# Performance work log

Hardware: AMD Instinct MI355X
Metric: run time of the kernel (lower is better)

The kernel has to match this reference:

```python
import jax, jax.numpy as jnp
import numpy as np

N_HEAD = 16
N_EMBD = 1024
HEAD_DIM = N_EMBD // N_HEAD  # 64
ROPE_BASE = 10000.0


def _rotary_cos_sin(T, dim, dtype=jnp.float32):
    # matches Rotary: inv_freq over even indices, cos/sin cached in bfloat16
    inv_freq = 1.0 / (ROPE_BASE ** (jnp.arange(0, dim, 2, dtype=jnp.float32) / dim))
    freqs = jnp.arange(T, dtype=jnp.float32)[:, None] * inv_freq[None, :]  # [T, dim/2]
    cos = jnp.cos(freqs).astype(jnp.bfloat16).astype(dtype)
    sin = jnp.sin(freqs).astype(jnp.bfloat16).astype(dtype)
    # shape [1, T, 1, dim/2] to broadcast over (B, T, H, d)
    return cos[None, :, None, :], sin[None, :, None, :]


def _apply_rotary(x, cos, sin):
    d = x.shape[3] // 2
    x1, x2 = x[..., :d], x[..., d:]
    y1 = x1 * cos + x2 * sin
    y2 = -x1 * sin + x2 * cos
    return jnp.concatenate([y1, y2], axis=3).astype(x.dtype)


def setup_inputs() -> dict:
    key = jax.random.key(0)
    ks = jax.random.split(key, 8)
    B, T, C = 2, 2048, N_EMBD
    scale = C ** -0.5  # realistic linear-layer init scale
    x = jax.random.normal(ks[0], (B, T, C), dtype=jnp.float32)
    Wq1 = jax.random.normal(ks[1], (C, C), dtype=jnp.float32) * scale
    Wk1 = jax.random.normal(ks[2], (C, C), dtype=jnp.float32) * scale
    Wq2 = jax.random.normal(ks[3], (C, C), dtype=jnp.float32) * scale
    Wk2 = jax.random.normal(ks[4], (C, C), dtype=jnp.float32) * scale
    Wv = jax.random.normal(ks[5], (C, C), dtype=jnp.float32) * scale
    Wout = jax.random.normal(ks[6], (C, C), dtype=jnp.float32) * scale
    return {"x": x, "Wq1": Wq1, "Wk1": Wk1, "Wq2": Wq2, "Wk2": Wk2, "Wv": Wv, "Wout": Wout}


def reference(x, Wq1, Wk1, Wq2, Wk2, Wv, Wout):
    B, T, C = x.shape
    H, D = N_HEAD, HEAD_DIM

    def proj(W):
        # torch nn.Linear(bias=False): y = x @ W.T
        return (x @ W.T).reshape(B, T, H, D)

    q1, k1 = proj(Wq1), proj(Wk1)
    q2, k2 = proj(Wq2), proj(Wk2)
    v = proj(Wv)

    cos, sin = _rotary_cos_sin(T, D, x.dtype)
    q1, k1 = _apply_rotary(q1, cos, sin), _apply_rotary(k1, cos, sin)
    q2, k2 = _apply_rotary(q2, cos, sin), _apply_rotary(k2, cos, sin)

    # two bilinear score maps, elementwise product, causal mask
    s1 = jnp.einsum('bqhd,bkhd->bhqk', q1, k1)  # [B,H,T,T]
    s2 = jnp.einsum('bqhd,bkhd->bhqk', q2, k2)
    causal = jnp.tril(jnp.ones((T, T), dtype=bool))
    pattern = jnp.where(causal[None, None], (s1 / D) * (s2 / D), 0.0)

    y = jnp.einsum('bhqk,bkhd->bqhd', pattern, v).reshape(B, T, C)
    return y @ Wout.T
```

## Files before the change

### kernel.cpp

```cpp
#include <hip/hip_runtime.h>
#include <hip/hip_bf16.h>
#include <math.h>

typedef __bf16 bf16;
typedef __bf16 bf16x8 __attribute__((ext_vector_type(8)));
typedef float  f32x4  __attribute__((ext_vector_type(4)));

#define NB    2
#define NT    2048
#define NH    16
#define ND    64
#define NC    1024
#define NBT   4096
#define NQT   32

#define AS1C(p) ((const __attribute__((address_space(1))) void*)(p))
#define AS3(p)  ((__attribute__((address_space(3))) void*)(p))

#define MFMA(a,b,c) __builtin_amdgcn_mfma_f32_16x16x32_bf16(a, b, c, 0, 0, 0)

struct WPtrs { const float* p[6]; };

__global__ void prep_kernel(const float* __restrict__ x, WPtrs w,
                            bf16* __restrict__ Xbf, bf16* __restrict__ Wcat,
                            float2* __restrict__ tbl)
{
    const int bid = blockIdx.x;
    if (bid < 4096) {
        const int i = (bid * 256 + threadIdx.x) * 4;
        float4 v = *reinterpret_cast<const float4*>(x + i);
        Xbf[i+0] = (bf16)v.x; Xbf[i+1] = (bf16)v.y;
        Xbf[i+2] = (bf16)v.z; Xbf[i+3] = (bf16)v.w;
    } else if (bid < 10240) {
        const int r   = bid - 4096;
        const int mat = r >> 10;
        const int off = ((r & 1023) * 256 + threadIdx.x) * 4;
        float4 v = *reinterpret_cast<const float4*>(w.p[mat] + off);
        bf16* d = Wcat + (size_t)mat * NC * NC + off;
        d[0] = (bf16)v.x; d[1] = (bf16)v.y; d[2] = (bf16)v.z; d[3] = (bf16)v.w;
    } else {
        const int i = (bid - 10240) * 256 + threadIdx.x;
        const int t = i >> 5, j = i & 31;
        float invf = 1.0f / powf(10000.0f, (float)j * (1.0f/32.0f));
        float fr = (float)t * invf;
        float2 cs;
        cs.x = (float)(bf16)cosf(fr);
        cs.y = (float)(bf16)sinf(fr);
        tbl[i] = cs;
    }
}

__global__ __launch_bounds__(256, 2)
void gemm_proj(const bf16* __restrict__ A, const bf16* __restrict__ Bw,
               bf16* __restrict__ qkv, const float2* __restrict__ tbl)
{
    __shared__ bf16 smem[2*16384];

    const int tid  = threadIdx.x;
    const int lane = tid & 63;
    const int w    = tid >> 6;
    const int wr   = w >> 1;
    const int wc   = w & 1;

    const int id  = blockIdx.x;
    const int swz = (id & 7) * 160 + (id >> 3);
    const int by  = swz / 40, bx = swz % 40;
    const int row0 = by * 128, col0 = bx * 128;

    const int lo  = lane & 15;
    const int hi  = lane >> 4;

    const int srow = tid >> 3;
    const int ssw  = ((tid & 7) ^ (srow & 7)) * 8;

    f32x4 acc[4][4] = {};

    auto stage = [&](int buf, int kt) {
        char* As = (char*)smem + buf*32768;
        char* Bs = As + 16384;
        #pragma unroll
        for (int i = 0; i < 4; ++i) {
            const unsigned loff = (unsigned)(i*4096 + w*1024);
            __builtin_amdgcn_global_load_lds(
                AS1C(A + (size_t)(row0 + i*32 + srow) * NC + kt + ssw),
                AS3(As + loff), 16, 0, 0);
            __builtin_amdgcn_global_load_lds(
                AS1C(Bw + (size_t)(col0 + i*32 + srow) * NC + kt + ssw),
                AS3(Bs + loff), 16, 0, 0);
        }
    };

    stage(0, 0);
    asm volatile("s_waitcnt vmcnt(0)" ::: "memory");
    __syncthreads();

    for (int kt = 0; kt < 16; ++kt) {
        const int cur = kt & 1;
        if (kt < 15) stage(cur ^ 1, (kt + 1) * 64);

        const char* As = (const char*)smem + cur*32768;
        const char* Bs = As + 16384;

        __builtin_amdgcn_s_setprio(1);
        #pragma unroll
        for (int ks = 0; ks < 2; ++ks) {
            bf16x8 af[4], bfr[4];
            #pragma unroll
            for (int m = 0; m < 4; ++m) {
                const int ar = wr*64 + m*16 + lo;
                af[m] = *reinterpret_cast<const bf16x8*>(
                    As + ar*128 + (((ks*4 + hi) ^ (lo & 7)) * 16));
            }
            #pragma unroll
            for (int n = 0; n < 4; ++n) {
                const int br = wc*64 + n*16 + lo;
                bfr[n] = *reinterpret_cast<const bf16x8*>(
                    Bs + br*128 + (((ks*4 + hi) ^ (lo & 7)) * 16));
            }
            #pragma unroll
            for (int m = 0; m < 4; ++m)
                #pragma unroll
                for (int n = 0; n < 4; ++n)
                    acc[m][n] = MFMA(af[m], bfr[n], acc[m][n]);
        }
        __builtin_amdgcn_s_setprio(0);

        asm volatile("s_waitcnt vmcnt(0)" ::: "memory");
        __syncthreads();
    }

    bf16* Ct = smem;
    const int p  = col0 >> 10;
    const int h0 = (col0 >> 6) & (NH-1);
    const int rb = hi * 4;

    if (p < 4) {
        const float qsc = (p == 0 || p == 2) ? 0.015625f : 1.0f;
        #pragma unroll
        for (int m = 0; m < 4; ++m)
            #pragma unroll
            for (int r = 0; r < 4; ++r) {
                const int rl = wr*64 + m*16 + rb + r;
                const int t  = (row0 + rl) & (NT-1);
                const unsigned key = ((unsigned)(rl >> 2) & 3) << 5;
                #pragma unroll
                for (int n = 0; n < 2; ++n) {
                    const int j = n*16 + lo;
                    float2 cs = tbl[t*32 + j];
                    float a1 = acc[m][n][r];
                    float a2 = acc[m][n+2][r];
                    const int c1 = wc*64 + j;
                    const int c2 = c1 + 32;
                    *(bf16*)((char*)Ct + (unsigned)(rl*256 + (((unsigned)c1*2) ^ key)))
                        = (bf16)((a1*cs.x + a2*cs.y) * qsc);
                    *(bf16*)((char*)Ct + (unsigned)(rl*256 + (((unsigned)c2*2) ^ key)))
                        = (bf16)((a2*cs.x - a1*cs.y) * qsc);
                }
            }
        __syncthreads();
        #pragma unroll
        for (int it = 0; it < 8; ++it) {
            const int chunk = it*256 + tid;
            const int rl = chunk >> 4;
            const int cc = chunk & 15;
            const unsigned key = ((unsigned)(rl >> 2) & 3) << 5;
            bf16x8 val = *reinterpret_cast<const bf16x8*>(
                (const char*)Ct + ((unsigned)rl*256 + (((unsigned)cc*16) ^ key)));
            const int rowg = row0 + rl;
            const int b = rowg >> 11;
            const int t = rowg & (NT-1);
            const int hh = h0 + (cc >> 3);
            const int d  = (cc & 7) * 8;
            *reinterpret_cast<bf16x8*>(
                qkv + ((((size_t)p*NB + b)*NH + hh)*NT + t)*ND + d) = val;
        }
    } else {
        #pragma unroll
        for (int m = 0; m < 4; ++m)
            #pragma unroll
            for (int r = 0; r < 4; ++r) {
                const int rl = wr*64 + m*16 + rb + r;
                #pragma unroll
                for (int n = 0; n < 4; ++n) {
                    const int c = wc*64 + n*16 + lo;
                    *(bf16*)((char*)Ct + (unsigned)(c*256 + (((unsigned)rl*2) ^ ((c&7)<<4))))
                        = (bf16)acc[m][n][r];
                }
            }
        __syncthreads();
        const int b  = row0 >> 11;
        const int t0 = row0 & (NT-1);
        #pragma unroll
        for (int it = 0; it < 8; ++it) {
            const int chunk = it*256 + tid;
            const int c   = chunk >> 4;
            const int tcc = chunk & 15;
            bf16x8 val = *reinterpret_cast<const bf16x8*>(
                (const char*)Ct + (unsigned)(c*256 + (((unsigned)tcc*16) ^ ((c&7)<<4))));
            const int hh = h0 + (c >> 6);
            const int d  = c & 63;
            *reinterpret_cast<bf16x8*>(
                qkv + (((size_t)4*NB + b)*NH + hh)*(size_t)NT*ND
                    + (size_t)d*NT + t0 + tcc*8) = val;
        }
    }
}

__global__ __launch_bounds__(256)
void gemm_out(const bf16* __restrict__ A, const bf16* __restrict__ Bw,
              float* __restrict__ Cp)
{
    __shared__ bf16 smem[2*16384];

    const int tid  = threadIdx.x;
    const int lane = tid & 63;
    const int w    = tid >> 6;
    const int wr   = w >> 1;
    const int wc   = w & 1;
    const int row0 = blockIdx.y * 128;
    const int col0 = blockIdx.x * 128;

    const int lo  = lane & 15;
    const int hi  = lane >> 4;

    const int srow = tid >> 3;
    const int ssw  = ((tid & 7) ^ (srow & 7)) * 8;

    f32x4 acc[4][4] = {};

    auto stage = [&](int buf, int kt) {
        char* As = (char*)smem + buf*32768;
        char* Bs = As + 16384;
        #pragma unroll
        for (int i = 0; i < 4; ++i) {
            const unsigned loff = (unsigned)(i*4096 + w*1024);
            __builtin_amdgcn_global_load_lds(
                AS1C(A + (size_t)(row0 + i*32 + srow) * NC + kt + ssw),
                AS3(As + loff), 16, 0, 0);
            __builtin_amdgcn_global_load_lds(
                AS1C(Bw + (size_t)(col0 + i*32 + srow) * NC + kt + ssw),
                AS3(Bs + loff), 16, 0, 0);
        }
    };

    stage(0, 0);
    asm volatile("s_waitcnt vmcnt(0)" ::: "memory");
    __syncthreads();

    for (int kt = 0; kt < 16; ++kt) {
        const int cur = kt & 1;
        if (kt < 15) stage(cur ^ 1, (kt + 1) * 64);

        const char* As = (const char*)smem + cur*32768;
        const char* Bs = As + 16384;

        __builtin_amdgcn_s_setprio(1);
        #pragma unroll
        for (int ks = 0; ks < 2; ++ks) {
            bf16x8 af[4], bfr[4];
            #pragma unroll
            for (int m = 0; m < 4; ++m) {
                const int ar = wr*64 + m*16 + lo;
                af[m] = *reinterpret_cast<const bf16x8*>(
                    As + ar*128 + (((ks*4 + hi) ^ (lo & 7)) * 16));
            }
            #pragma unroll
            for (int n = 0; n < 4; ++n) {
                const int br = wc*64 + n*16 + lo;
                bfr[n] = *reinterpret_cast<const bf16x8*>(
                    Bs + br*128 + (((ks*4 + hi) ^ (lo & 7)) * 16));
            }
            #pragma unroll
            for (int m = 0; m < 4; ++m)
                #pragma unroll
                for (int n = 0; n < 4; ++n)
                    acc[m][n] = MFMA(af[m], bfr[n], acc[m][n]);
        }
        __builtin_amdgcn_s_setprio(0);

        asm volatile("s_waitcnt vmcnt(0)" ::: "memory");
        __syncthreads();
    }

    const int rb = hi * 4;
    #pragma unroll
    for (int m = 0; m < 4; ++m)
        #pragma unroll
        for (int n = 0; n < 4; ++n)
            #pragma unroll
            for (int r = 0; r < 4; ++r) {
                int row = row0 + wr*64 + m*16 + rb + r;
                int col = col0 + wc*64 + n*16 + lo;
                Cp[(size_t)row * NC + col] = acc[m][n][r];
            }
}

__global__ __launch_bounds__(256, 2)
void attn_kernel(const bf16* __restrict__ qkv, bf16* __restrict__ Y)
{
    __shared__ bf16 K1s[3*4096];
    __shared__ bf16 K2s[3*4096];
    __shared__ bf16 Vts[3*4096];
    __shared__ bf16 Pl [4][1024];

    const int tid  = threadIdx.x;
    const int lane = tid & 63;
    const int w    = tid >> 6;

    const int lin  = blockIdx.x;
    const int xcd  = lin & 7;
    const int slot = lin >> 3;
    const int pair = xcd * 4 + (slot >> 4);
    const int qa   = slot & 15;
    const int h    = pair >> 1;
    const int b    = pair & 1;
    const int qb   = NQT - 1 - qa;

    const size_t plane = (size_t)NB * NH * NT * ND;
    const size_t bh    = ((size_t)b * NH + h) * (size_t)NT * ND;
    const bf16* Q1 = qkv + 0*plane + bh;
    const bf16* K1 = qkv + 1*plane + bh;
    const bf16* Q2 = qkv + 2*plane + bh;
    const bf16* K2 = qkv + 3*plane + bh;
    const bf16* V  = qkv + 4*plane + bh;

    const int lo  = lane & 15;
    const int hi  = lane >> 4;
    const int hi8 = hi * 8;

    bf16x8 q1fa[2], q2fa[2], q1fb[2], q2fb[2];
    #pragma unroll
    for (int dd = 0; dd < 2; ++dd) {
        const size_t ra  = (size_t)(qa*64 + w*16 + lo) * ND + dd*32 + hi8;
        const size_t rbq = (size_t)(qb*64 + w*16 + lo) * ND + dd*32 + hi8;
        q1fa[dd] = *reinterpret_cast<const bf16x8*>(Q1 + ra);
        q2fa[dd] = *reinterpret_cast<const bf16x8*>(Q2 + ra);
        q1fb[dd] = *reinterpret_cast<const bf16x8*>(Q1 + rbq);
        q2fb[dd] = *reinterpret_cast<const bf16x8*>(Q2 + rbq);
    }

    f32x4 yacca[4] = {}, yaccb[4] = {};

    const int srow = tid >> 3;
    const int ssw  = ((tid & 7) ^ (srow & 7)) * 8;

    auto stageK = [&](int buf, int k0) {
        #pragma unroll
        for (int i = 0; i < 2; ++i) {
            const unsigned loff = (unsigned)(buf*8192 + i*4096 + w*1024);
            __builtin_amdgcn_global_load_lds(
                AS1C(K1 + (size_t)(k0 + i*32 + srow) * ND + ssw),
                AS3((char*)K1s + loff), 16, 0, 0);
            __builtin_amdgcn_global_load_lds(
                AS1C(K2 + (size_t)(k0 + i*32 + srow) * ND + ssw),
                AS3((char*)K2s + loff), 16, 0, 0);
        }
    };
    auto stageVT = [&](int buf, int k0) {
        #pragma unroll
        for (int i = 0; i < 2; ++i) {
            const int inst = w*2 + i;
            const int d    = inst*8 + (lane >> 3);
            const int sc   = ((lane & 7) ^ ((lane >> 3) & 7)) * 8;
            __builtin_amdgcn_global_load_lds(
                AS1C(V + (size_t)d * NT + k0 + sc),
                AS3((char*)Vts + (unsigned)(buf*8192 + inst*1024)), 16, 0, 0);
        }
    };

    stageK(0, 0);  stageVT(0, 0);
    stageK(1, 64); stageVT(1, 64);

    int cur = 0;
    for (int kt = 0; kt <= qb; ++kt) {
        if (kt < qb) asm volatile("s_waitcnt vmcnt(6)" ::: "memory");
        else         asm volatile("s_waitcnt vmcnt(0)" ::: "memory");
        __syncthreads();
        if (kt + 2 <= qb) {
            int nx = cur + 2; if (nx >= 3) nx -= 3;
            stageK(nx, (kt + 2) * 64);
            stageVT(nx, (kt + 2) * 64);
        }

        const bool doA = (kt <= qa);
        const bf16* K1b = K1s + cur*4096;
        const bf16* K2b = K2s + cur*4096;
        const char* Vb  = (const char*)Vts + cur*8192;

        f32x4 s1a[4] = {}, s2a[4] = {}, s1b[4] = {}, s2b[4] = {};
        __builtin_amdgcn_s_setprio(1);
        #pragma unroll
        for (int dd = 0; dd < 2; ++dd)
            #pragma unroll
            for (int sub = 0; sub < 4; ++sub) {
                const unsigned kb = (unsigned)((sub*16 + lo)*128 + (((dd*4 + hi) ^ (lo & 7)) * 16));
                bf16x8 k1f = *reinterpret_cast<const bf16x8*>((const char*)K1b + kb);
                bf16x8 k2f = *reinterpret_cast<const bf16x8*>((const char*)K2b + kb);
                s1b[sub] = MFMA(q1fb[dd], k1f, s1b[sub]);
                s2b[sub] = MFMA(q2fb[dd], k2f, s2b[sub]);
                if (doA) {
                    s1a[sub] = MFMA(q1fa[dd], k1f, s1a[sub]);
                    s2a[sub] = MFMA(q2fa[dd], k2f, s2a[sub]);
                }
            }
        __builtin_amdgcn_s_setprio(0);

        #define COMBINE(S1, S2, DIAG)                                                  \
            _Pragma("unroll")                                                          \
            for (int sub = 0; sub < 4; ++sub)                                          \
                _Pragma("unroll")                                                      \
                for (int r = 0; r < 4; ++r) {                                          \
                    const int row = hi*4 + r;                                          \
                    const int col = sub*16 + lo;                                       \
                    const unsigned byte = (unsigned)(row*128 + (((col>>3) ^ (row&7))*16) + (col&7)*2); \
                    float pv = S1[sub][r] * S2[sub][r];                                \
                    if (DIAG && col > w*16 + row) pv = 0.0f;                           \
                    *(bf16*)((char*)Pl[w] + byte) = (bf16)pv;                          \
                }

        if (kt == qb) { COMBINE(s1b, s2b, true) } else { COMBINE(s1b, s2b, false) }
        asm volatile("s_waitcnt lgkmcnt(0)" ::: "memory");
        __builtin_amdgcn_sched_barrier(0);

        bf16x8 vfr[2][4];
        __builtin_amdgcn_s_setprio(1);
        #pragma unroll
        for (int ks = 0; ks < 2; ++ks) {
            const unsigned pby = (unsigned)(lo*128 + (((ks*4 + hi) ^ (lo & 7)) * 16));
            bf16x8 pfb = *reinterpret_cast<const bf16x8*>((const char*)Pl[w] + pby);
            #pragma unroll
            for (int n = 0; n < 4; ++n) {
                const unsigned vby = (unsigned)((n*16 + lo)*128 + (((ks*4 + hi) ^ (lo & 7)) * 16));
                vfr[ks][n] = *reinterpret_cast<const bf16x8*>(Vb + vby);
                yaccb[n] = MFMA(pfb, vfr[ks][n], yaccb[n]);
            }
        }
        __builtin_amdgcn_s_setprio(0);

        if (doA) {
            asm volatile("s_waitcnt lgkmcnt(0)" ::: "memory");
            __builtin_amdgcn_sched_barrier(0);
            if (kt == qa) { COMBINE(s1a, s2a, true) } else { COMBINE(s1a, s2a, false) }
            asm volatile("s_waitcnt lgkmcnt(0)" ::: "memory");
            __builtin_amdgcn_sched_barrier(0);
            __builtin_amdgcn_s_setprio(1);
            #pragma unroll
            for (int ks = 0; ks < 2; ++ks) {
                const unsigned pby = (unsigned)(lo*128 + (((ks*4 + hi) ^ (lo & 7)) * 16));
                bf16x8 pfa = *reinterpret_cast<const bf16x8*>((const char*)Pl[w] + pby);
                #pragma unroll
                for (int n = 0; n < 4; ++n)
                    yacca[n] = MFMA(pfa, vfr[ks][n], yacca[n]);
            }
            __builtin_amdgcn_s_setprio(0);
        }
        #undef COMBINE

        cur += 1; if (cur >= 3) cur -= 3;
    }

    auto writeOut = [&](int q0, const f32x4* ya) {
        #pragma unroll
        for (int n = 0; n < 4; ++n)
            #pragma unroll
            for (int r = 0; r < 4; ++r) {
                const int row = hi*4 + r;
                const int col = n*16 + lo;
                const unsigned byte = (unsigned)(row*128 + (((col>>3) ^ (row&7))*16) + (col&7)*2);
                *(bf16*)((char*)Pl[w] + byte) = (bf16)ya[n][r];
            }
        asm volatile("s_waitcnt lgkmcnt(0)" ::: "memory");
        __builtin_amdgcn_sched_barrier(0);
        #pragma unroll
        for (int pass = 0; pass < 2; ++pass) {
            const int idx = pass*64 + lane;
            const int row = idx >> 3;
            const int cc  = idx & 7;
            bf16x8 val = *reinterpret_cast<const bf16x8*>(
                (const char*)Pl[w] + row*128 + ((cc ^ (row&7))*16));
            const int t = q0 + w*16 + row;
            const int c = h*ND + cc*8;
            *reinterpret_cast<bf16x8*>(Y + ((size_t)b*NT + t)*NC + c) = val;
        }
    };
    writeOut(qa*64, yacca);
    writeOut(qb*64, yaccb);
}

extern "C" void kernel_launch(void* const* d_in, const int* in_sizes, int n_in,
                              void* d_out, int out_size, void* d_ws, size_t ws_size,
                              hipStream_t stream)
{
    const float* x = (const float*)d_in[0];

    char* ws = (char*)d_ws;
    bf16*   Xbf   = (bf16*)ws;
    bf16*   Wcat  = (bf16*)(ws + (size_t)NBT*NC*2);
    bf16*   QKV   = (bf16*)(ws + (size_t)NBT*NC*2 + (size_t)6*NC*NC*2);
    bf16*   Ybf   = (bf16*)((char*)QKV + (size_t)5*NBT*NC*2);
    float2* tbl   = (float2*)((char*)Ybf + (size_t)NBT*NC*2);
    bf16*   Woutb = Wcat + (size_t)5*NC*NC;

    WPtrs wp;
    wp.p[0] = (const float*)d_in[1]; wp.p[1] = (const float*)d_in[2];
    wp.p[2] = (const float*)d_in[3]; wp.p[3] = (const float*)d_in[4];
    wp.p[4] = (const float*)d_in[5]; wp.p[5] = (const float*)d_in[6];

    prep_kernel<<<dim3(10496), 256, 0, stream>>>(x, wp, Xbf, Wcat, tbl);

    gemm_proj<<<dim3(1280), 256, 0, stream>>>(Xbf, Wcat, QKV, tbl);
    attn_kernel<<<dim3(512), 256, 0, stream>>>(QKV, Ybf);
    gemm_out<<<dim3(NC/128, NBT/128), 256, 0, stream>>>(Ybf, Woutb, (float*)d_out);
}
```

Before: 146.8 us.

## Deepen GEMM pipelines to four K=32 stages and halve gemm_out tile width

Both GEMMs now stage K in 32-wide slices across a 4-deep ring of LDS buffers, keeping two loads in flight. Each iteration uses a partial vmcnt wait and one barrier, where before it did a full drain plus a syncthreads every 64-wide step. gemm_out also drops to 128x64 tiles, doubling its grid from 256 to 512 blocks to fill more CUs. The cost is more barriers per K, a smaller swizzle that may raise LDS bank conflicts, and more A-tile reloads in gemm_out.

```diff
diff --git a/kernel.cpp b/kernel.cpp
--- a/kernel.cpp
+++ b/kernel.cpp
@@ -54,7 +54,7 @@
 void gemm_proj(const bf16* __restrict__ A, const bf16* __restrict__ Bw,
                bf16* __restrict__ qkv, const float2* __restrict__ tbl)
 {
-    __shared__ bf16 smem[2*16384];
+    __shared__ bf16 smem[4*8192];
 
     const int tid  = threadIdx.x;
     const int lane = tid & 63;
@@ -70,64 +70,59 @@
     const int lo  = lane & 15;
     const int hi  = lane >> 4;
 
-    const int srow = tid >> 3;
-    const int ssw  = ((tid & 7) ^ (srow & 7)) * 8;
+    const int hrow = w*16 + (lane >> 2);
+    const int hcol = ((lane & 3) ^ ((lane >> 3) & 3)) * 8;
 
     f32x4 acc[4][4] = {};
 
-    auto stage = [&](int buf, int kt) {
-        char* As = (char*)smem + buf*32768;
-        char* Bs = As + 16384;
-        #pragma unroll
-        for (int i = 0; i < 4; ++i) {
-            const unsigned loff = (unsigned)(i*4096 + w*1024);
+    auto stageHalf = [&](int s) {
+        char* base = (char*)smem + (s & 3) * 16384;
+        const int k0 = s * 32;
+        #pragma unroll
+        for (int i = 0; i < 2; ++i) {
             __builtin_amdgcn_global_load_lds(
-                AS1C(A + (size_t)(row0 + i*32 + srow) * NC + kt + ssw),
-                AS3(As + loff), 16, 0, 0);
+                AS1C(A + (size_t)(row0 + i*64 + hrow) * NC + k0 + hcol),
+                AS3(base + i*4096 + w*1024), 16, 0, 0);
             __builtin_amdgcn_global_load_lds(
-                AS1C(Bw + (size_t)(col0 + i*32 + srow) * NC + kt + ssw),
-                AS3(Bs + loff), 16, 0, 0);
+                AS1C(Bw + (size_t)(col0 + i*64 + hrow) * NC + k0 + hcol),
+                AS3(base + 8192 + i*4096 + w*1024), 16, 0, 0);
         }
     };
 
-    stage(0, 0);
-    asm volatile("s_waitcnt vmcnt(0)" ::: "memory");
+    stageHalf(0);
+    stageHalf(1);
+
+    const int csw = (lo >> 1) & 3;
+    for (int s = 0; s < 32; ++s) {
+        if (s < 31) asm volatile("s_waitcnt vmcnt(4)" ::: "memory");
+        else        asm volatile("s_waitcnt vmcnt(0)" ::: "memory");
+        __builtin_amdgcn_s_barrier();
+        asm volatile("" ::: "memory");
+        if (s + 2 < 32) stageHalf(s + 2);
+
+        const char* As = (const char*)smem + (s & 3) * 16384;
+        const char* Bs = As + 8192;
+
+        bf16x8 af[4], bfr[4];
+        #pragma unroll
+        for (int m = 0; m < 4; ++m) {
+            const int ar = wr*64 + m*16 + lo;
+            af[m] = *reinterpret_cast<const bf16x8*>(As + ar*64 + ((hi ^ csw) * 16));
+        }
+        #pragma unroll
+        for (int n = 0; n < 4; ++n) {
+            const int br = wc*64 + n*16 + lo;
+            bfr[n] = *reinterpret_cast<const bf16x8*>(Bs + br*64 + ((hi ^ csw) * 16));
+        }
+        __builtin_amdgcn_s_setprio(1);
+        #pragma unroll
+        for (int m = 0; m < 4; ++m)
+            #pragma unroll
+            for (int n = 0; n < 4; ++n)
+                acc[m][n] = MFMA(af[m], bfr[n], acc[m][n]);
+        __builtin_amdgcn_s_setprio(0);
+    }
     __syncthreads();
-
-    for (int kt = 0; kt < 16; ++kt) {
-        const int cur = kt & 1;
-        if (kt < 15) stage(cur ^ 1, (kt + 1) * 64);
-
-        const char* As = (const char*)smem + cur*32768;
-        const char* Bs = As + 16384;
-
-        __builtin_amdgcn_s_setprio(1);
-        #pragma unroll
-        for (int ks = 0; ks < 2; ++ks) {
-            bf16x8 af[4], bfr[4];
-            #pragma unroll
-            for (int m = 0; m < 4; ++m) {
-                const int ar = wr*64 + m*16 + lo;
-                af[m] = *reinterpret_cast<const bf16x8*>(
-                    As + ar*128 + (((ks*4 + hi) ^ (lo & 7)) * 16));
-            }
-            #pragma unroll
-            for (int n = 0; n < 4; ++n) {
-                const int br = wc*64 + n*16 + lo;
-                bfr[n] = *reinterpret_cast<const bf16x8*>(
-                    Bs + br*128 + (((ks*4 + hi) ^ (lo & 7)) * 16));
-            }
-            #pragma unroll
-            for (int m = 0; m < 4; ++m)
-                #pragma unroll
-                for (int n = 0; n < 4; ++n)
-                    acc[m][n] = MFMA(af[m], bfr[n], acc[m][n]);
-        }
-        __builtin_amdgcn_s_setprio(0);
-
-        asm volatile("s_waitcnt vmcnt(0)" ::: "memory");
-        __syncthreads();
-    }
 
     bf16* Ct = smem;
     const int p  = col0 >> 10;
@@ -210,7 +205,7 @@
 void gemm_out(const bf16* __restrict__ A, const bf16* __restrict__ Bw,
               float* __restrict__ Cp)
 {
-    __shared__ bf16 smem[2*16384];
+    __shared__ bf16 smem[4*6144];
 
     const int tid  = threadIdx.x;
     const int lane = tid & 63;
@@ -218,79 +213,72 @@
     const int wr   = w >> 1;
     const int wc   = w & 1;
     const int row0 = blockIdx.y * 128;
-    const int col0 = blockIdx.x * 128;
+    const int col0 = blockIdx.x * 64;
 
     const int lo  = lane & 15;
     const int hi  = lane >> 4;
 
-    const int srow = tid >> 3;
-    const int ssw  = ((tid & 7) ^ (srow & 7)) * 8;
-
-    f32x4 acc[4][4] = {};
-
-    auto stage = [&](int buf, int kt) {
-        char* As = (char*)smem + buf*32768;
-        char* Bs = As + 16384;
-        #pragma unroll
-        for (int i = 0; i < 4; ++i) {
-            const unsigned loff = (unsigned)(i*4096 + w*1024);
+    const int hrow = w*16 + (lane >> 2);
+    const int hcol = ((lane & 3) ^ ((lane >> 3) & 3)) * 8;
+
+    f32x4 acc[4][2] = {};
+
+    auto stageHalf = [&](int s) {
+        char* base = (char*)smem + (s & 3) * 12288;
+        const int k0 = s * 32;
+        #pragma unroll
+        for (int i = 0; i < 2; ++i)
             __builtin_amdgcn_global_load_lds(
-                AS1C(A + (size_t)(row0 + i*32 + srow) * NC + kt + ssw),
-                AS3(As + loff), 16, 0, 0);
-            __builtin_amdgcn_global_load_lds(
-                AS1C(Bw + (size_t)(col0 + i*32 + srow) * NC + kt + ssw),
-                AS3(Bs + loff), 16, 0, 0);
-        }
+                AS1C(A + (size_t)(row0 + i*64 + hrow) * NC + k0 + hcol),
+                AS3(base + i*4096 + w*1024), 16, 0, 0);
+        __builtin_amdgcn_global_load_lds(
+            AS1C(Bw + (size_t)(col0 + hrow) * NC + k0 + hcol),
+            AS3(base + 8192 + w*1024), 16, 0, 0);
     };
 
-    stage(0, 0);
-    asm volatile("s_waitcnt vmcnt(0)" ::: "memory");
-    __syncthreads();
-
-    for (int kt = 0; kt < 16; ++kt) {
-        const int cur = kt & 1;
-        if (kt < 15) stage(cur ^ 1, (kt + 1) * 64);
-
-        const char* As = (const char*)smem + cur*32768;
-        const char* Bs = As + 16384;
-
+    stageHalf(0);
+    stageHalf(1);
+
+    const int csw = (lo >> 1) & 3;
+    for (int s = 0; s < 32; ++s) {
+        if (s < 31) asm volatile("s_waitcnt vmcnt(3)" ::: "memory");
+        else        asm volatile("s_waitcnt vmcnt(0)" ::: "memory");
+        __builtin_amdgcn_s_barrier();
+        asm volatile("" ::: "memory");
+        if (s + 2 < 32) stageHalf(s + 2);
+
+        const char* As = (const char*)smem + (s & 3) * 12288;
+        const char* Bs = As + 8192;
+
+        bf16x8 af[4], bfr[2];
+        #pragma unroll
+        for (int m = 0; m < 4; ++m) {
+            const int ar = wr*64 + m*16 + lo;
+            af[m] = *reinterpret_cast<const bf16x8*>(As + ar*64 + ((hi ^ csw) * 16));
+        }
+        #pragma unroll
+        for (int n = 0; n < 2; ++n) {
+            const int br = wc*32 + n*16 + lo;
+            bfr[n] = *reinterpret_cast<const bf16x8*>(Bs + br*64 + ((hi ^ csw) * 16));
+        }
         __builtin_amdgcn_s_setprio(1);
         #pragma unroll
-        for (int ks = 0; ks < 2; ++ks) {
-            bf16x8 af[4], bfr[4];
-            #pragma unroll
-            for (int m = 0; m < 4; ++m) {
-                const int ar = wr*64 + m*16 + lo;
-                af[m] = *reinterpret_cast<const bf16x8*>(
-                    As + ar*128 + (((ks*4 + hi) ^ (lo & 7)) * 16));
-            }
-            #pragma unroll
-            for (int n = 0; n < 4; ++n) {
-                const int br = wc*64 + n*16 + lo;
-                bfr[n] = *reinterpret_cast<const bf16x8*>(
-                    Bs + br*128 + (((ks*4 + hi) ^ (lo & 7)) * 16));
-            }
-            #pragma unroll
-            for (int m = 0; m < 4; ++m)
-                #pragma unroll
-                for (int n = 0; n < 4; ++n)
-                    acc[m][n] = MFMA(af[m], bfr[n], acc[m][n]);
-        }
+        for (int m = 0; m < 4; ++m)
+            #pragma unroll
+            for (int n = 0; n < 2; ++n)
+                acc[m][n] = MFMA(af[m], bfr[n], acc[m][n]);
         __builtin_amdgcn_s_setprio(0);
-
-        asm volatile("s_waitcnt vmcnt(0)" ::: "memory");
-        __syncthreads();
     }
 
     const int rb = hi * 4;
     #pragma unroll
     for (int m = 0; m < 4; ++m)
         #pragma unroll
-        for (int n = 0; n < 4; ++n)
+        for (int n = 0; n < 2; ++n)
             #pragma unroll
             for (int r = 0; r < 4; ++r) {
                 int row = row0 + wr*64 + m*16 + rb + r;
-                int col = col0 + wc*64 + n*16 + lo;
+                int col = col0 + wc*32 + n*16 + lo;
                 Cp[(size_t)row * NC + col] = acc[m][n][r];
             }
 }
@@ -510,5 +498,5 @@
 
     gemm_proj<<<dim3(1280), 256, 0, stream>>>(Xbf, Wcat, QKV, tbl);
     attn_kernel<<<dim3(512), 256, 0, stream>>>(QKV, Ybf);
-    gemm_out<<<dim3(NC/128, NBT/128), 256, 0, stream>>>(Ybf, Woutb, (float*)d_out);
+    gemm_out<<<dim3(NC/64, NBT/128), 256, 0, stream>>>(Ybf, Woutb, (float*)d_out);
 }
```

Measured after the change: 146.2 us. About the same (-0.4%).
